# Kernel optimization log

Measured on AMD Instinct MI355X. Metric: run time of the kernel, lower is better.

Reference implementation:

```python
import jax, jax.numpy as jnp
import numpy as np

D_MODEL = 1024
N, L = 4, 2048


def setup_inputs() -> dict:
    key = jax.random.key(0)
    ks = jax.random.split(key, 8)
    s = 0.1
    return {
        "X": jax.random.normal(ks[0], (N, L, D_MODEL), dtype=jnp.float32),
        "W_Q1": jax.random.normal(ks[1], (D_MODEL, D_MODEL), dtype=jnp.float32) * s,
        "W_K1": jax.random.normal(ks[2], (D_MODEL, D_MODEL), dtype=jnp.float32) * s,
        "W_V1": jax.random.normal(ks[3], (D_MODEL, D_MODEL), dtype=jnp.float32) * s,
        "W_Q2": jax.random.normal(ks[4], (D_MODEL, D_MODEL), dtype=jnp.float32) * s,
        "W_K2": jax.random.normal(ks[5], (D_MODEL, D_MODEL), dtype=jnp.float32) * s,
        "W_V2": jax.random.normal(ks[6], (D_MODEL, D_MODEL), dtype=jnp.float32) * s,
        "W_O": jax.random.normal(ks[7], (D_MODEL, 1), dtype=jnp.float32) * s,
        "b_O": jnp.zeros((1, 1), dtype=jnp.float32),
    }


def _attn_block(H, W_Q, W_K, W_V):
    # H: (N, L, D); single-head scaled dot-product attention
    Q = jnp.einsum('nld,dk->nlk', H, W_Q)
    K = jnp.einsum('nld,dk->nlk', H, W_K)
    V = jnp.einsum('nld,dk->nlk', H, W_V)
    scale = jnp.sqrt(jnp.asarray(Q.shape[-1], Q.dtype))
    scores = jnp.einsum('nqd,nkd->nqk', Q, K) / scale  # (N, L, L)
    attn = jax.nn.softmax(scores, axis=-1)
    return jnp.einsum('nqk,nkd->nqd', attn, V)


def reference(X, W_Q1, W_K1, W_V1, W_Q2, W_K2, W_V2, W_O, b_O):
    H1 = _attn_block(X, W_Q1, W_K1, W_V1)
    H2 = _attn_block(H1, W_Q2, W_K2, W_V2)
    pooled = jnp.mean(H2, axis=1)            # (N, D)
    logits = pooled @ W_O + b_O              # (N, 1)
    return jax.nn.sigmoid(logits).squeeze(-1)  # (N,)
```

## Files before the change

### kernel.cpp

```cpp
#include <hip/hip_runtime.h>
#include <hip/hip_bf16.h>
#include <cstdint>


#define DEVFN __device__ __forceinline__

typedef __attribute__((ext_vector_type(8))) short bf16x8;
typedef __attribute__((ext_vector_type(8))) _Float16 f16x8;
typedef __attribute__((ext_vector_type(4))) float f32x4;
typedef unsigned short u16;

DEVFN u16 f2bf(float f) {
    uint32_t x = __float_as_uint(f);
    x += 0x7fffu + ((x >> 16) & 1u);
    return (u16)(x >> 16);
}
DEVFN float bf2f(u16 u) { return __uint_as_float(((uint32_t)u) << 16); }

DEVFN void gload_lds16(const void* g, void* l) {
    __builtin_amdgcn_global_load_lds(
        (const __attribute__((address_space(1))) void*)g,
        (__attribute__((address_space(3))) void*)l, 16, 0, 0);
}

#define MFMA16 __builtin_amdgcn_mfma_f32_16x16x32_bf16

template<int EPI>
__global__ __launch_bounds__(256, 4) void gemmk(
    const u16* __restrict__ A, long long aStride,
    const u16* __restrict__ B, long long bStride,
    void* __restrict__ out0, void* __restrict__ out1,
    const float* __restrict__ zrow, long long cStride,
    int M, int N, int K, int lda, int ldb, int ldc, float scale)
{
    constexpr int ASEC  = 128 * 32;
    constexpr int BUFSZ = ASEC + 128 * 32;
    constexpr int NU    = 4;

    __shared__ __align__(16) u16 L[2 * BUFSZ];
    const int tid  = threadIdx.x;
    const int wave = tid >> 6, lane = tid & 63;

    const int gx = gridDim.x, gy = gridDim.y;
    const int nwg = gx * gy * gridDim.z;
    int flat = (blockIdx.z * gy + blockIdx.y) * gx + blockIdx.x;
    flat = (flat & 7) * (nwg >> 3) + (flat >> 3);
    const int bx = flat % gx, by = (flat / gx) % gy, bz = flat / (gx * gy);

    const u16* pA = A + (size_t)bz * aStride;
    const u16* pB = B + (size_t)bz * bStride;
    const int m0 = by * 128, n0 = bx * 128;

    const u16* src[NU];
    int dst[NU];
#pragma unroll
    for (int q = 0; q < 2; q++) {
        const int s = q * 256 + tid, row = s >> 2, c = (s & 3) ^ ((row >> 1) & 3);
        src[q]     = pA + (size_t)(m0 + row) * lda + c * 8;
        dst[q]     = q * 2048 + wave * 512;
        src[2 + q] = pB + (size_t)(n0 + row) * ldb + c * 8;
        dst[2 + q] = ASEC + q * 2048 + wave * 512;
    }

    const int fr = lane & 15, ch = lane >> 4;
    const int wr = (wave >> 1) * 64, wc = (wave & 1) * 64;

    const int NT = K >> 5;

#pragma unroll
    for (int u = 0; u < NU; u++) { gload_lds16(src[u], &L[dst[u]]); src[u] += 32; }
    __syncthreads();

    f32x4 acc[4][4] = {};
    int cur = 0;

    for (int kt = 0; kt < NT; ++kt) {
        const int cOff = cur * BUFSZ;
        const int sOff = BUFSZ - cOff;
        if (kt + 1 < NT) {
#pragma unroll
            for (int u = 0; u < NU; u++) { gload_lds16(src[u], &L[sOff + dst[u]]); src[u] += 32; }
        }

        bf16x8 ah[4], bh[4];
#pragma unroll
        for (int i = 0; i < 4; i++) {
            const int r = wr + i * 16 + fr;
            ah[i] = *(const bf16x8*)&L[cOff + r * 32 + ((ch ^ ((r >> 1) & 3)) << 3)];
        }
#pragma unroll
        for (int j = 0; j < 4; j++) {
            const int r = wc + j * 16 + fr;
            bh[j] = *(const bf16x8*)&L[cOff + ASEC + r * 32 + ((ch ^ ((r >> 1) & 3)) << 3)];
        }

#pragma unroll
        for (int i = 0; i < 4; i++)
#pragma unroll
            for (int j = 0; j < 4; j++)
                acc[i][j] = MFMA16(ah[i], bh[j], acc[i][j], 0, 0, 0);

        __syncthreads();
        cur ^= 1;
    }

    if constexpr (EPI == 5) {
#pragma unroll
        for (int i = 0; i < 4; i++)
#pragma unroll
            for (int r = 0; r < 4; r++) {
                const int rowb = m0 + wr + i * 16 + ch * 4 + r;
                float s = 0.f;
#pragma unroll
                for (int j = 0; j < 4; j++) {
                    const int col = n0 + wc + j * 16 + fr;
                    const float e = __expf(acc[i][j][r] * scale - 60.f);
                    s += e;
                    ((u16*)out0)[(size_t)bz * cStride + (size_t)rowb * ldc + col] = f2bf(e);
                }
                s += __shfl_xor(s, 1, 16);
                s += __shfl_xor(s, 2, 16);
                s += __shfl_xor(s, 4, 16);
                s += __shfl_xor(s, 8, 16);
                if (fr == 0)
                    ((float*)out1)[((size_t)bz * 2048 + rowb) * 32 + ((n0 + wc) >> 6)] = s;
            }
    } else if constexpr (EPI == 6) {
#pragma unroll
        for (int i = 0; i < 4; i++)
#pragma unroll
            for (int r = 0; r < 4; r++) {
                const int row = m0 + wr + i * 16 + ch * 4 + r;
                const size_t grow = (size_t)bz * 2048 + row;
                float zp = zrow[grow * 32 + 2 * fr] + zrow[grow * 32 + 2 * fr + 1];
                zp += __shfl_xor(zp, 1, 16);
                zp += __shfl_xor(zp, 2, 16);
                zp += __shfl_xor(zp, 4, 16);
                zp += __shfl_xor(zp, 8, 16);
                const float zi = 1.f / zp;
#pragma unroll
                for (int j = 0; j < 4; j++) {
                    const int col = n0 + wc + j * 16 + fr;
                    ((u16*)out0)[(size_t)bz * cStride + (size_t)row * ldc + col] =
                        f2bf(acc[i][j][r] * zi);
                }
            }
    } else {
#pragma unroll
        for (int i = 0; i < 4; i++)
#pragma unroll
            for (int j = 0; j < 4; j++)
#pragma unroll
                for (int r = 0; r < 4; r++) {
                    const int row = m0 + wr + i * 16 + (lane >> 4) * 4 + r;
                    const int col = n0 + wc + j * 16 + (lane & 15);
                    const float v = acc[i][j][r] * scale;
                    if constexpr (EPI == 3) {
                        ((u16*)out0)[(size_t)bz * cStride + (size_t)row * ldc + col] = f2bf(v);
                    } else {
                        ((_Float16*)out0)[(size_t)bz * cStride + (size_t)row * ldc + col] =
                            (_Float16)v;
                    }
                }
    }
}

__global__ __launch_bounds__(256, 4) void gemm_tv(
    const u16* __restrict__ Xb, const u16* __restrict__ Mt1,
    const u16* __restrict__ Wv1T, u16* __restrict__ Tb, u16* __restrict__ Vtb)
{
    constexpr int ASEC  = 128 * 32;
    constexpr int BUFSZ = ASEC + 128 * 32;
    constexpr int NU    = 4;

    __shared__ __align__(16) u16 L[2 * BUFSZ];
    const int tid  = threadIdx.x;
    const int wave = tid >> 6, lane = tid & 63;

    int flat = blockIdx.x;
    flat = (flat & 7) * 128 + (flat >> 3);
    const int op = flat & 1, t = flat >> 1;
    const u16* pA;
    const u16* pB;
    u16* outp;
    int m0, n0, ldc;
    if (op == 0) {
        pA = Xb;  pB = Mt1;  outp = Tb;  ldc = 1024;
        m0 = (t >> 3) * 128; n0 = (t & 7) * 128;
    } else {
        pA = Wv1T; pB = Xb;  outp = Vtb; ldc = 8192;
        m0 = (t >> 6) * 128; n0 = (t & 63) * 128;
    }

    const u16* src[NU];
    int dst[NU];
#pragma unroll
    for (int q = 0; q < 2; q++) {
        const int s = q * 256 + tid, row = s >> 2, c = (s & 3) ^ ((row >> 1) & 3);
        src[q]     = pA + (size_t)(m0 + row) * 1024 + c * 8;
        dst[q]     = q * 2048 + wave * 512;
        src[2 + q] = pB + (size_t)(n0 + row) * 1024 + c * 8;
        dst[2 + q] = ASEC + q * 2048 + wave * 512;
    }

    const int fr = lane & 15, ch = lane >> 4;
    const int wr = (wave >> 1) * 64, wc = (wave & 1) * 64;

#pragma unroll
    for (int u = 0; u < NU; u++) { gload_lds16(src[u], &L[dst[u]]); src[u] += 32; }
    __syncthreads();

    f32x4 acc[4][4] = {};
    int cur = 0;

    for (int kt = 0; kt < 32; ++kt) {
        const int cOff = cur * BUFSZ;
        const int sOff = BUFSZ - cOff;
        if (kt + 1 < 32) {
#pragma unroll
            for (int u = 0; u < NU; u++) { gload_lds16(src[u], &L[sOff + dst[u]]); src[u] += 32; }
        }

        bf16x8 ah[4], bh[4];
#pragma unroll
        for (int i = 0; i < 4; i++) {
            const int r = wr + i * 16 + fr;
            ah[i] = *(const bf16x8*)&L[cOff + r * 32 + ((ch ^ ((r >> 1) & 3)) << 3)];
        }
#pragma unroll
        for (int j = 0; j < 4; j++) {
            const int r = wc + j * 16 + fr;
            bh[j] = *(const bf16x8*)&L[cOff + ASEC + r * 32 + ((ch ^ ((r >> 1) & 3)) << 3)];
        }

#pragma unroll
        for (int i = 0; i < 4; i++)
#pragma unroll
            for (int j = 0; j < 4; j++)
                acc[i][j] = MFMA16(ah[i], bh[j], acc[i][j], 0, 0, 0);

        __syncthreads();
        cur ^= 1;
    }

#pragma unroll
    for (int i = 0; i < 4; i++)
#pragma unroll
        for (int j = 0; j < 4; j++)
#pragma unroll
            for (int r = 0; r < 4; r++) {
                const int row = m0 + wr + i * 16 + (lane >> 4) * 4 + r;
                const int col = n0 + wc + j * 16 + (lane & 15);
                outp[(size_t)row * ldc + col] = f2bf(acc[i][j][r]);
            }
}

__global__ __launch_bounds__(256) void prep_all(
    const float* __restrict__ X,
    const float* __restrict__ W0, const float* __restrict__ W1,
    const float* __restrict__ W2, const float* __restrict__ W3,
    const float* __restrict__ Wv1, const float* __restrict__ Wv2,
    const float* __restrict__ wO,
    u16* __restrict__ Xb, u16* __restrict__ Wcat,
    u16* __restrict__ Wv1T, float* __restrict__ wv)
{
    const int blk = blockIdx.x, tid = threadIdx.x;
    __shared__ float t[64][65];

    if (blk < 8192) {
        const size_t i = ((size_t)blk * 256 + tid) * 4;
        const float4 v = *(const float4*)&X[i];
        ushort4 h;
        h.x = f2bf(v.x); h.y = f2bf(v.y); h.z = f2bf(v.z); h.w = f2bf(v.w);
        *(ushort4*)&Xb[i] = h;
    } else if (blk < 12288) {
        const int w = (blk - 8192) >> 10, ib = (blk - 8192) & 1023;
        const float* W = (w == 0) ? W0 : (w == 1) ? W1 : (w == 2) ? W2 : W3;
        u16* o = Wcat + (size_t)w * 1048576;
        const size_t i = ((size_t)ib * 256 + tid) * 4;
        const float4 v = *(const float4*)&W[i];
        ushort4 h;
        h.x = f2bf(v.x); h.y = f2bf(v.y); h.z = f2bf(v.z); h.w = f2bf(v.w);
        *(ushort4*)&o[i] = h;
    } else if (blk < 12544) {
        const int tb = blk - 12288;
        const int r0 = (tb >> 4) * 64, c0 = (tb & 15) * 64;
#pragma unroll
        for (int it = 0; it < 16; it++) {
            const int idx = it * 256 + tid, rr = idx >> 6, cc = idx & 63;
            t[rr][cc] = Wv1[(size_t)(r0 + rr) * 1024 + (c0 + cc)];
        }
        __syncthreads();
#pragma unroll
        for (int it = 0; it < 16; it++) {
            const int idx = it * 256 + tid, nn = idx >> 6, kk = idx & 63;
            Wv1T[(size_t)(c0 + nn) * 1024 + (r0 + kk)] = f2bf(t[kk][nn]);
        }
    } else {
        const int d = (blk - 12544) * 16 + (tid >> 4);
        const int lx = tid & 15;
        const float* row = Wv2 + (size_t)d * 1024;
        float s = 0.f;
#pragma unroll
        for (int it = 0; it < 16; it++) {
            const int j = it * 64 + lx * 4;
            const float4 a = *(const float4*)&row[j];
            const float4 w = *(const float4*)&wO[j];
            s += a.x * w.x + a.y * w.y + a.z * w.z + a.w * w.w;
        }
#pragma unroll
        for (int o = 8; o; o >>= 1) s += __shfl_xor(s, o, 16);
        if (lx == 0) wv[d] = s;
    }
}

__global__ __launch_bounds__(256) void mid_head(
    const _Float16* __restrict__ S, float* __restrict__ part,
    const u16* __restrict__ H1, const float* __restrict__ wv,
    float* __restrict__ u)
{
    const int blk = blockIdx.x, tid = threadIdx.x;
    __shared__ float redm[4], reds[4];

    if (blk < 512) {
        const int b = blk >> 7, chunk = blk & 127;
        const _Float16* Sb = S + (size_t)b * (2048 * 2048) + (size_t)chunk * 16 * 2048;
        float acc[8] = {};

        for (int r = 0; r < 16; r++) {
            const _Float16* row = Sb + (size_t)r * 2048;
            const f16x8 hv = *(const f16x8*)&row[tid * 8];
            float v[8];
#pragma unroll
            for (int j = 0; j < 8; j++) v[j] = (float)hv[j];

            float m = v[0];
#pragma unroll
            for (int j = 1; j < 8; j++) m = fmaxf(m, v[j]);
            for (int o = 32; o; o >>= 1) m = fmaxf(m, __shfl_xor(m, o));
            if ((tid & 63) == 0) redm[tid >> 6] = m;
            __syncthreads();
            m = fmaxf(fmaxf(redm[0], redm[1]), fmaxf(redm[2], redm[3]));

            float e[8], s = 0.f;
#pragma unroll
            for (int j = 0; j < 8; j++) { e[j] = __expf(v[j] - m); s += e[j]; }
            for (int o = 32; o; o >>= 1) s += __shfl_xor(s, o);
            if ((tid & 63) == 0) reds[tid >> 6] = s;
            __syncthreads();
            const float inv = 1.f / (reds[0] + reds[1] + reds[2] + reds[3]);
#pragma unroll
            for (int j = 0; j < 8; j++) acc[j] += e[j] * inv;
            __syncthreads();
        }

        float* p = part + ((size_t)(b * 128 + chunk)) * 2048;
#pragma unroll
        for (int j = 0; j < 8; j++) p[tid * 8 + j] = acc[j];
    } else {
        const int r = (blk - 512) * 16 + (tid >> 4);
        const int lx = tid & 15;
        const u16* row = H1 + (size_t)r * 1024;
        float s = 0.f;
#pragma unroll
        for (int it = 0; it < 8; it++) {
            const int d = it * 128 + lx * 8;
            const bf16x8 h = *(const bf16x8*)&row[d];
#pragma unroll
            for (int j = 0; j < 8; j++) s += bf2f((u16)h[j]) * wv[d + j];
        }
#pragma unroll
        for (int o = 8; o; o >>= 1) s += __shfl_xor(s, o, 16);
        if (lx == 0) u[r] = s;
    }
}

__global__ __launch_bounds__(256) void tail2(
    const float* __restrict__ part, float* __restrict__ csum)
{
    const int blk = blockIdx.x, tid = threadIdx.x;
    const int b = blk >> 5;
    const int kl = tid & 63;
    const int k = (blk & 31) * 64 + kl;
    const int cg = tid >> 6;
    float s = 0.f;
#pragma unroll 4
    for (int c = 0; c < 32; c++)
        s += part[((size_t)(b * 128 + cg * 32 + c)) * 2048 + k];
    __shared__ float red[4][64];
    red[cg][kl] = s;
    __syncthreads();
    if (cg == 0)
        csum[b * 2048 + k] = red[0][kl] + red[1][kl] + red[2][kl] + red[3][kl];
}

__global__ void head_final(const float* __restrict__ csum,
                           const float* __restrict__ u,
                           const float* __restrict__ bO, float* __restrict__ out)
{
    const int b = threadIdx.x >> 6, lane = threadIdx.x & 63;
    float s = 0.f;
    for (int k = lane; k < 2048; k += 64)
        s += csum[b * 2048 + k] * u[b * 2048 + k];
    for (int o = 32; o; o >>= 1) s += __shfl_xor(s, o);
    if (lane == 0) {
        const float logit = s * (1.f / 2048.f) + bO[0];
        out[b] = 1.f / (1.f + __expf(-logit));
    }
}

extern "C" void kernel_launch(void* const* d_in, const int* in_sizes, int n_in,
                              void* d_out, int out_size, void* d_ws, size_t ws_size,
                              hipStream_t stream)
{
    const float* X   = (const float*)d_in[0];
    const float* Wq1 = (const float*)d_in[1];
    const float* Wk1 = (const float*)d_in[2];
    const float* Wv1 = (const float*)d_in[3];
    const float* Wq2 = (const float*)d_in[4];
    const float* Wk2 = (const float*)d_in[5];
    const float* Wv2 = (const float*)d_in[6];
    const float* WO  = (const float*)d_in[7];
    const float* bO  = (const float*)d_in[8];
    float* out = (float*)d_out;

    uint8_t* ws = (uint8_t*)d_ws;
    const size_t MB = 1ull << 20;
    u16* Xb   = (u16*)(ws + 0);
    u16* Tb   = (u16*)(ws + 32 * MB);
    float* part  = (float*)(ws + 80 * MB);
    float* csum  = (float*)(ws + 85 * MB);
    float* wv    = (float*)(ws + 86 * MB);
    float* ud    = (float*)(ws + 87 * MB);
    float* Zpart = (float*)(ws + 88 * MB);
    u16* Vtb  = (u16*)(ws + 96 * MB);
    u16* Wcat = (u16*)(ws + 128 * MB);
    u16* Eb   = (u16*)(ws + 152 * MB);
    _Float16* Sh = (_Float16*)(ws + 152 * MB);

    auto Wslot = [&](int i) { return Wcat + (size_t)i * 1048576; };

    prep_all<<<12608, 256, 0, stream>>>(
        X, Wq1, Wq2, Wk1, Wk2, Wv1, Wv2, WO, Xb, Wcat, Wslot(5), wv);
    gemmk<3><<<dim3(8, 8, 2), 256, 0, stream>>>(
        Wslot(2), 1048576, Wslot(0), 1048576, Wslot(4), nullptr, nullptr,
        2 * 1048576LL, 1024, 1024, 1024, 1024, 1024, 1024, 1.f);

    const long long LD2 = 2048LL * 1024;
    const long long EST = 2048LL * 2048;

    gemm_tv<<<1024, 256, 0, stream>>>(Xb, Wslot(4), Wslot(5), Tb, Vtb);
    gemmk<5><<<dim3(16, 16, 4), 256, 0, stream>>>(
        Tb, LD2, Xb, LD2, Eb, Zpart, nullptr, EST,
        2048, 2048, 1024, 1024, 1024, 2048, 0.03125f);
    gemmk<6><<<dim3(8, 16, 4), 256, 0, stream>>>(
        Eb, EST, Vtb, 2048, Xb, nullptr, Zpart, LD2,
        2048, 1024, 2048, 2048, 8192, 1024, 1.f);

    gemmk<3><<<dim3(8, 64, 1), 256, 0, stream>>>(
        Xb, 0, Wslot(6), 0, Tb, nullptr, nullptr, 0,
        8192, 1024, 1024, 1024, 1024, 1024, 1.f);
    gemmk<8><<<dim3(16, 16, 4), 256, 0, stream>>>(
        Tb, LD2, Xb, LD2, Sh, nullptr, nullptr, EST,
        2048, 2048, 1024, 1024, 1024, 2048, 0.03125f);

    mid_head<<<1024, 256, 0, stream>>>(Sh, part, Xb, wv, ud);
    tail2<<<128, 256, 0, stream>>>(part, csum);
    head_final<<<1, 256, 0, stream>>>(csum, ud, bO, out);
}
```

Measured before the change: 266.6 us.

## Triple-buffer GEMM LDS pipeline with vmcnt waits; fold head dot into tail2

Both GEMM kernels move from double to triple LDS buffering. They issue loads two k-tiles ahead and replace __syncthreads with an explicit s_waitcnt vmcnt plus a raw barrier, so a global load has more time to arrive before its tile is needed. In exchange, LDS per block grows from 32KB to 48KB and occupancy drops from 4 to 3 blocks per CU. The tail2 kernel now multiplies by u and reduces per block, so head_final only sums 32 partials per batch instead of doing a 2048-long dot product.

```diff
diff --git a/kernel.cpp b/kernel.cpp
--- a/kernel.cpp
+++ b/kernel.cpp
@@ -26,7 +26,7 @@
 #define MFMA16 __builtin_amdgcn_mfma_f32_16x16x32_bf16
 
 template<int EPI>
-__global__ __launch_bounds__(256, 4) void gemmk(
+__global__ __launch_bounds__(256, 3) void gemmk(
     const u16* __restrict__ A, long long aStride,
     const u16* __restrict__ B, long long bStride,
     void* __restrict__ out0, void* __restrict__ out1,
@@ -37,7 +37,7 @@
     constexpr int BUFSZ = ASEC + 128 * 32;
     constexpr int NU    = 4;
 
-    __shared__ __align__(16) u16 L[2 * BUFSZ];
+    __shared__ __align__(16) u16 L[3 * BUFSZ];
     const int tid  = threadIdx.x;
     const int wave = tid >> 6, lane = tid & 63;
 
@@ -69,15 +69,19 @@
 
 #pragma unroll
     for (int u = 0; u < NU; u++) { gload_lds16(src[u], &L[dst[u]]); src[u] += 32; }
-    __syncthreads();
+#pragma unroll
+    for (int u = 0; u < NU; u++) { gload_lds16(src[u], &L[BUFSZ + dst[u]]); src[u] += 32; }
+    asm volatile("s_waitcnt vmcnt(4)" ::: "memory");
+    __builtin_amdgcn_s_barrier();
+    __builtin_amdgcn_sched_barrier(0);
 
     f32x4 acc[4][4] = {};
-    int cur = 0;
+    int cIdx = 0, sIdx = 2;
 
     for (int kt = 0; kt < NT; ++kt) {
-        const int cOff = cur * BUFSZ;
-        const int sOff = BUFSZ - cOff;
-        if (kt + 1 < NT) {
+        const int cOff = cIdx * BUFSZ;
+        if (kt + 2 < NT) {
+            const int sOff = sIdx * BUFSZ;
 #pragma unroll
             for (int u = 0; u < NU; u++) { gload_lds16(src[u], &L[sOff + dst[u]]); src[u] += 32; }
         }
@@ -100,8 +104,14 @@
             for (int j = 0; j < 4; j++)
                 acc[i][j] = MFMA16(ah[i], bh[j], acc[i][j], 0, 0, 0);
 
-        __syncthreads();
-        cur ^= 1;
+        if (kt + 1 < NT) {
+            if (kt + 2 < NT) asm volatile("s_waitcnt vmcnt(4)" ::: "memory");
+            else             asm volatile("s_waitcnt vmcnt(0)" ::: "memory");
+            __builtin_amdgcn_s_barrier();
+            __builtin_amdgcn_sched_barrier(0);
+        }
+        cIdx = (cIdx == 2) ? 0 : cIdx + 1;
+        sIdx = (sIdx == 2) ? 0 : sIdx + 1;
     }
 
     if constexpr (EPI == 5) {
@@ -165,7 +175,7 @@
     }
 }
 
-__global__ __launch_bounds__(256, 4) void gemm_tv(
+__global__ __launch_bounds__(256, 3) void gemm_tv(
     const u16* __restrict__ Xb, const u16* __restrict__ Mt1,
     const u16* __restrict__ Wv1T, u16* __restrict__ Tb, u16* __restrict__ Vtb)
 {
@@ -173,7 +183,7 @@
     constexpr int BUFSZ = ASEC + 128 * 32;
     constexpr int NU    = 4;
 
-    __shared__ __align__(16) u16 L[2 * BUFSZ];
+    __shared__ __align__(16) u16 L[3 * BUFSZ];
     const int tid  = threadIdx.x;
     const int wave = tid >> 6, lane = tid & 63;
 
@@ -208,15 +218,19 @@
 
 #pragma unroll
     for (int u = 0; u < NU; u++) { gload_lds16(src[u], &L[dst[u]]); src[u] += 32; }
-    __syncthreads();
+#pragma unroll
+    for (int u = 0; u < NU; u++) { gload_lds16(src[u], &L[BUFSZ + dst[u]]); src[u] += 32; }
+    asm volatile("s_waitcnt vmcnt(4)" ::: "memory");
+    __builtin_amdgcn_s_barrier();
+    __builtin_amdgcn_sched_barrier(0);
 
     f32x4 acc[4][4] = {};
-    int cur = 0;
+    int cIdx = 0, sIdx = 2;
 
     for (int kt = 0; kt < 32; ++kt) {
-        const int cOff = cur * BUFSZ;
-        const int sOff = BUFSZ - cOff;
-        if (kt + 1 < 32) {
+        const int cOff = cIdx * BUFSZ;
+        if (kt + 2 < 32) {
+            const int sOff = sIdx * BUFSZ;
 #pragma unroll
             for (int u = 0; u < NU; u++) { gload_lds16(src[u], &L[sOff + dst[u]]); src[u] += 32; }
         }
@@ -239,8 +253,14 @@
             for (int j = 0; j < 4; j++)
                 acc[i][j] = MFMA16(ah[i], bh[j], acc[i][j], 0, 0, 0);
 
-        __syncthreads();
-        cur ^= 1;
+        if (kt + 1 < 32) {
+            if (kt + 2 < 32) asm volatile("s_waitcnt vmcnt(4)" ::: "memory");
+            else             asm volatile("s_waitcnt vmcnt(0)" ::: "memory");
+            __builtin_amdgcn_s_barrier();
+            __builtin_amdgcn_sched_barrier(0);
+        }
+        cIdx = (cIdx == 2) ? 0 : cIdx + 1;
+        sIdx = (sIdx == 2) ? 0 : sIdx + 1;
     }
 
 #pragma unroll
@@ -376,7 +396,8 @@
 }
 
 __global__ __launch_bounds__(256) void tail2(
-    const float* __restrict__ part, float* __restrict__ csum)
+    const float* __restrict__ part, const float* __restrict__ u,
+    float* __restrict__ partial)
 {
     const int blk = blockIdx.x, tid = threadIdx.x;
     const int b = blk >> 5;
@@ -390,22 +411,24 @@
     __shared__ float red[4][64];
     red[cg][kl] = s;
     __syncthreads();
-    if (cg == 0)
-        csum[b * 2048 + k] = red[0][kl] + red[1][kl] + red[2][kl] + red[3][kl];
-}
-
-__global__ void head_final(const float* __restrict__ csum,
-                           const float* __restrict__ u,
+    if (cg == 0) {
+        float v = (red[0][kl] + red[1][kl] + red[2][kl] + red[3][kl])
+                  * u[b * 2048 + k];
+        for (int o = 32; o; o >>= 1) v += __shfl_xor(v, o);
+        if (kl == 0) partial[blk] = v;
+    }
+}
+
+__global__ void head_final(const float* __restrict__ partial,
                            const float* __restrict__ bO, float* __restrict__ out)
 {
-    const int b = threadIdx.x >> 6, lane = threadIdx.x & 63;
-    float s = 0.f;
-    for (int k = lane; k < 2048; k += 64)
-        s += csum[b * 2048 + k] * u[b * 2048 + k];
-    for (int o = 32; o; o >>= 1) s += __shfl_xor(s, o);
-    if (lane == 0) {
-        const float logit = s * (1.f / 2048.f) + bO[0];
-        out[b] = 1.f / (1.f + __expf(-logit));
+    const int t = threadIdx.x;
+    float v = partial[t];
+#pragma unroll
+    for (int o = 16; o; o >>= 1) v += __shfl_xor(v, o);
+    if ((t & 31) == 0) {
+        const float logit = v * (1.f / 2048.f) + bO[0];
+        out[t >> 5] = 1.f / (1.f + __expf(-logit));
     }
 }
 
@@ -428,11 +451,11 @@
     const size_t MB = 1ull << 20;
     u16* Xb   = (u16*)(ws + 0);
     u16* Tb   = (u16*)(ws + 32 * MB);
-    float* part  = (float*)(ws + 80 * MB);
-    float* csum  = (float*)(ws + 85 * MB);
-    float* wv    = (float*)(ws + 86 * MB);
-    float* ud    = (float*)(ws + 87 * MB);
-    float* Zpart = (float*)(ws + 88 * MB);
+    float* part    = (float*)(ws + 80 * MB);
+    float* partial = (float*)(ws + 85 * MB);
+    float* wv      = (float*)(ws + 86 * MB);
+    float* ud      = (float*)(ws + 87 * MB);
+    float* Zpart   = (float*)(ws + 88 * MB);
     u16* Vtb  = (u16*)(ws + 96 * MB);
     u16* Wcat = (u16*)(ws + 128 * MB);
     u16* Eb   = (u16*)(ws + 152 * MB);
@@ -465,6 +488,6 @@
         2048, 2048, 1024, 1024, 1024, 2048, 0.03125f);
 
     mid_head<<<1024, 256, 0, stream>>>(Sh, part, Xb, wv, ud);
-    tail2<<<128, 256, 0, stream>>>(part, csum);
-    head_final<<<1, 256, 0, stream>>>(csum, ud, bO, out);
-}
+    tail2<<<128, 256, 0, stream>>>(part, ud, partial);
+    head_final<<<1, 128, 0, stream>>>(partial, bO, out);
+}
```

Measured after the change: 261.0 us. 2.1% less time.
